# Optimization experiments

Hardware: AMD Instinct MI355X
Metric: run time of the kernel (lower is better)

## Reference

```python
import jax, jax.numpy as jnp
import numpy as np

DS = 16                      # downsample
DEPTH_MIN, DEPTH_MAX = 1.0, 60.0
XB = (-51.2, 51.2, 0.4)      # bev_x_bound
YB = (-51.2, 51.2, 0.4)      # bev_y_bound
ZB = (-5.0, 3.0)             # bev_z_bound (min, max)
BEV_H = int((YB[1] - YB[0]) / YB[2])   # 256
BEV_W = int((XB[1] - XB[0]) / XB[2])   # 256


def setup_inputs() -> dict:
    key = jax.random.key(0)
    k1, k2 = jax.random.split(key)
    B, N, C, H, W, D = 2, 6, 128, 16, 44, 64
    feat = jax.random.normal(k1, (B, N, C, H, W), dtype=jnp.float32)
    # depth distribution: softmax over depth bins (as a real LSS depth head produces)
    depth = jax.nn.softmax(jax.random.normal(k2, (B, N, D, H, W), dtype=jnp.float32), axis=2)
    # intrinsics chosen so that after the module's internal K scaling the frustum
    # rays actually spread over the BEV grid (non-degenerate valid mask)
    K = np.array([[2.0, 0.0, 1.34], [0.0, 2.0, 0.47], [0.0, 0.0, 1.0]], dtype=np.float32)
    intrinsics = np.broadcast_to(K, (B, N, 3, 3)).copy()
    # 6 cameras looking outward: cam(x right, y down, z fwd) -> ego(x fwd, y left, z up), yawed
    base = np.array([[0, 0, 1], [-1, 0, 0], [0, -1, 0]], dtype=np.float32)
    Es = []
    for yaw in np.linspace(0.0, 2.0 * np.pi, N, endpoint=False):
        c, s = np.cos(yaw), np.sin(yaw)
        Rz = np.array([[c, -s, 0], [s, c, 0], [0, 0, 1]], dtype=np.float32)
        E = np.eye(4, dtype=np.float32)
        E[:3, :3] = Rz @ base
        E[:3, 3] = [1.0 * c, 1.0 * s, 1.5]
        Es.append(E)
    extrinsics = np.broadcast_to(np.stack(Es), (B, N, 4, 4)).copy()
    return {
        "feat": feat,
        "depth": depth,
        "intrinsics": jnp.asarray(intrinsics),
        "extrinsics": jnp.asarray(extrinsics),
        "img_h": 256,
        "img_w": 704,
    }


def _forward(feat, depth, intrinsics, extrinsics, img_h, img_w):
    B, N, C, H, W = feat.shape
    D = depth.shape[2]
    dt = feat.dtype
    # frustum (D,H,W) of pixel coords u,v and metric depth d
    dbins = jnp.linspace(DEPTH_MIN, DEPTH_MAX, D).astype(dt)
    yy, xx = jnp.meshgrid(jnp.arange(H, dtype=dt), jnp.arange(W, dtype=dt), indexing='ij')
    u = jnp.broadcast_to(xx[None], (D, H, W)).reshape(-1)
    v = jnp.broadcast_to(yy[None], (D, H, W)).reshape(-1)
    d = jnp.broadcast_to(dbins[:, None, None], (D, H, W)).reshape(-1)
    # intrinsics scaled exactly as the torch module does (rows 0,1 scaled)
    scale_x = W / (img_w / DS)
    scale_y = H / (img_h / DS)
    rs = jnp.array([DS / scale_x, DS / scale_y, 1.0], dtype=dt)
    K = intrinsics * rs[:, None]            # (B,N,3,3)
    Kinv = jnp.linalg.inv(K)
    uvd = jnp.stack([u * d, v * d, d], axis=-1)     # (P,3), P = D*H*W
    pc = jnp.einsum('bnij,pj->bnpi', Kinv, uvd)     # camera-frame points
    R = extrinsics[..., :3, :3]
    t = extrinsics[..., :3, 3]
    pts = jnp.einsum('bnij,bnpj->bnpi', R, pc) + t[:, :, None, :]   # (B,N,P,3) ego
    pts = pts.reshape(B, -1, 3)                     # (B, N*P, 3)
    # depth-lift: feat (B,N,C,H,W) x depth (B,N,D,H,W) -> (B, N*D*H*W, C)
    lifted = (feat[:, :, :, None] * depth[:, :, None]).transpose(0, 1, 3, 4, 5, 2).reshape(B, -1, C)
    # voxelize (torch .long() truncates toward zero; so does astype here)
    xi = ((pts[..., 0] - XB[0]) / XB[2]).astype(jnp.int32)
    yi = ((pts[..., 1] - YB[0]) / YB[2]).astype(jnp.int32)
    valid = (xi >= 0) & (xi < BEV_W) & (yi >= 0) & (yi < BEV_H) & \
            (pts[..., 2] >= ZB[0]) & (pts[..., 2] <= ZB[1])
    idx = jnp.where(valid, yi * BEV_W + xi, 0)      # invalid -> cell 0 with zeroed value
    vals = lifted * valid[..., None].astype(dt)
    seg = lambda val, i: jax.ops.segment_sum(val, i, num_segments=BEV_H * BEV_W)
    bev = jax.vmap(seg)(vals, idx)                  # (B, cells, C)
    cnt = jax.vmap(seg)(valid.astype(dt), idx)      # (B, cells)
    bev = bev.transpose(0, 2, 1).reshape(B, C, BEV_H, BEV_W)
    cnt = cnt.reshape(B, 1, BEV_H, BEV_W)
    return bev / (cnt + 1e-5)


def reference(feat, depth, intrinsics, extrinsics, img_h, img_w):
    return _forward(feat, depth, intrinsics, extrinsics, img_h, img_w)
```

## Files before the change

kernel.cpp:

```cpp
#include <hip/hip_runtime.h>
#include <hip/hip_bf16.h>

#define Bc 2
#define Nc 6
#define Cc 128
#define Hc 16
#define Wc 44
#define Dc 64
#define HWc (Hc*Wc)
#define BNc (Bc*Nc)
#define NRAY (Nc*HWc)
#define NPTS (Bc*Nc*Dc*HWc)
#define NCOL (BNc*Wc*Dc)
#define BEV_W 256
#define BEV_H 256
#define BEV_HW (BEV_W*BEV_H)
#define NSEG (Bc*BEV_HW)
#define NSCANB 512
#define NGRP (NSEG/16)
#define GB  768
#define GW  (GB*4)
#define ZB  256
#define ZW  (ZB*4)

#define OFF_KI    0
#define OFF_DB    512
#define OFF_CNTC  1024
#define OFF_CNTP  (OFF_CNTC + 524288)
#define OFF_OFFS  (OFF_CNTP + 524288)
#define OFF_BSUM  (OFF_OFFS + 524288)
#define OFF_E8    (OFF_BSUM + 4096)
#define OFF_PK2   (OFF_E8   + 270336)
#define OFF_FT    (OFF_PK2  + 270336)
#define OFF_DT    (OFF_FT   + 4325376)
#define WS_BIG    77337600
#define OFF_FIDX  OFF_FT
#define OFF_FCNT  OFF_CNTC

__device__ __forceinline__ void setup_into(int tid, const float* __restrict__ intr,
                                           const int* __restrict__ p_imgh,
                                           const int* __restrict__ p_imgw,
                                           float* Ki, float* db) {
    if (tid < Dc) {
        double v = 1.0 + (double)tid * (59.0 / 63.0);
        db[tid] = (tid == Dc - 1) ? 60.0f : (float)v;
    }
    if (tid >= BNc) return;
    double img_h = (double)p_imgh[0];
    double img_w = (double)p_imgw[0];
    double scale_x = (double)Wc / (img_w / 16.0);
    double scale_y = (double)Hc / (img_h / 16.0);
    float rs0 = (float)(16.0 / scale_x);
    float rs1 = (float)(16.0 / scale_y);
    float rs2 = 1.0f;
    const float* K = intr + tid * 9;
    float k0 = __fmul_rn(K[0], rs0), k1 = __fmul_rn(K[1], rs0), k2 = __fmul_rn(K[2], rs0);
    float k3 = __fmul_rn(K[3], rs1), k4 = __fmul_rn(K[4], rs1), k5 = __fmul_rn(K[5], rs1);
    float k6 = __fmul_rn(K[6], rs2), k7 = __fmul_rn(K[7], rs2), k8 = __fmul_rn(K[8], rs2);
    float c0 = __fsub_rn(__fmul_rn(k4,k8), __fmul_rn(k5,k7));
    float c1 = __fsub_rn(__fmul_rn(k3,k8), __fmul_rn(k5,k6));
    float c2 = __fsub_rn(__fmul_rn(k3,k7), __fmul_rn(k4,k6));
    float det = __fadd_rn(__fsub_rn(__fmul_rn(k0,c0), __fmul_rn(k1,c1)), __fmul_rn(k2,c2));
    float* o = Ki + tid * 9;
    o[0] = __fdiv_rn(c0, det);
    o[1] = __fdiv_rn(__fsub_rn(__fmul_rn(k2,k7), __fmul_rn(k1,k8)), det);
    o[2] = __fdiv_rn(__fsub_rn(__fmul_rn(k1,k5), __fmul_rn(k2,k4)), det);
    o[3] = __fdiv_rn(__fsub_rn(__fmul_rn(k5,k6), __fmul_rn(k3,k8)), det);
    o[4] = __fdiv_rn(__fsub_rn(__fmul_rn(k0,k8), __fmul_rn(k2,k6)), det);
    o[5] = __fdiv_rn(__fsub_rn(__fmul_rn(k2,k3), __fmul_rn(k0,k5)), det);
    o[6] = __fdiv_rn(c2, det);
    o[7] = __fdiv_rn(__fsub_rn(__fmul_rn(k1,k6), __fmul_rn(k0,k7)), det);
    o[8] = __fdiv_rn(__fsub_rn(__fmul_rn(k0,k4), __fmul_rn(k1,k3)), det);
}

__global__ void k_setup(const float* __restrict__ intr, const float* __restrict__ extr,
                        const int* __restrict__ p_imgh, const int* __restrict__ p_imgw,
                        float* __restrict__ Ki, float* __restrict__ db) {
    setup_into(threadIdx.x, intr, p_imgh, p_imgw, Ki, db);
}

__device__ __forceinline__ int classify_point(int gid, const float* Ki_all,
                                              const float* db, const float* extr) {
    int p   = gid % HWc;
    int tmp = gid / HWc;
    int d   = tmp % Dc;
    int bn  = tmp / Dc;
    int w = p % Wc, h = p / Wc;
    float dd = db[d];
    float ud = __fmul_rn((float)w, dd);
    float vd = __fmul_rn((float)h, dd);
    const float* Ki = Ki_all + bn * 9;
    float pcx = fmaf(Ki[2], dd, fmaf(Ki[1], vd, __fmul_rn(Ki[0], ud)));
    float pcy = fmaf(Ki[5], dd, fmaf(Ki[4], vd, __fmul_rn(Ki[3], ud)));
    float pcz = fmaf(Ki[8], dd, fmaf(Ki[7], vd, __fmul_rn(Ki[6], ud)));
    const float* E = extr + bn * 16;
    float px = __fadd_rn(fmaf(E[2],  pcz, fmaf(E[1], pcy, __fmul_rn(E[0], pcx))), E[3]);
    float py = __fadd_rn(fmaf(E[6],  pcz, fmaf(E[5], pcy, __fmul_rn(E[4], pcx))), E[7]);
    float pz = __fadd_rn(fmaf(E[10], pcz, fmaf(E[9], pcy, __fmul_rn(E[8], pcx))), E[11]);
    float fx = __fdiv_rn(__fsub_rn(px, -51.2f), 0.4f);
    float fy = __fdiv_rn(__fsub_rn(py, -51.2f), 0.4f);
    int xi = (int)fx;
    int yi = (int)fy;
    bool valid = (xi >= 0) && (xi < BEV_W) && (yi >= 0) && (yi < BEV_H)
              && (pz >= -5.0f) && (pz <= 3.0f);
    return valid ? (yi * BEV_W + xi) : -1;
}

__device__ __forceinline__ void scan_bsum(int tid, const int* __restrict__ bsum,
                                          int* sB, int* su, int* pEtotS) {
    int2 v2 = ((const int2*)bsum)[tid];
    int s = v2.x + v2.y;
    su[tid] = s;
    __syncthreads();
    for (int st = 1; st < 256; st <<= 1) {
        int t2 = (tid >= st) ? su[tid - st] : 0;
        __syncthreads();
        su[tid] += t2;
        __syncthreads();
    }
    int base = su[tid] - s;
    sB[2 * tid]     = base;
    sB[2 * tid + 1] = base + v2.x;
    if (tid == 255) *pEtotS = base + s;
    __syncthreads();
}

__global__ __launch_bounds__(256) void k_countC(const float* __restrict__ intr,
                                                const float* __restrict__ extr,
                                                const int* __restrict__ p_imgh,
                                                const int* __restrict__ p_imgw,
                                                const float* __restrict__ feat,
                                                const float* __restrict__ depth,
                                                int* __restrict__ cntC,
                                                int* __restrict__ cntP,
                                                int2* __restrict__ pk2,
                                                float* __restrict__ ft,
                                                float* __restrict__ dT) {
    __shared__ float sKi[BNc * 9];
    __shared__ float sDb[Dc];
    __shared__ float shmem[11534];
    int tid = threadIdx.x;
    setup_into(tid, intr, p_imgh, p_imgw, sKi, sDb);
    __syncthreads();

    if (blockIdx.x < NCOL / 256) {
        int col = blockIdx.x * 256 + tid;
        int bn  = col / (Wc * Dc);
        int rem = col % (Wc * Dc);
        int w = rem / Dc, d = rem % Dc;
        const float* Ki = sKi + bn * 9;
        const float* E  = extr + bn * 16;
        float dd = sDb[d];
        float ud = __fmul_rn((float)w, dd);
        float vd0  = __fmul_rn(0.0f, dd);
        float pcx0 = fmaf(Ki[2], dd, fmaf(Ki[1], vd0, __fmul_rn(Ki[0], ud)));
        float pcy0 = fmaf(Ki[5], dd, fmaf(Ki[4], vd0, __fmul_rn(Ki[3], ud)));
        float pcz0 = fmaf(Ki[8], dd, fmaf(Ki[7], vd0, __fmul_rn(Ki[6], ud)));
        float px = __fadd_rn(fmaf(E[2], pcz0, fmaf(E[1], pcy0, __fmul_rn(E[0], pcx0))), E[3]);
        float py = __fadd_rn(fmaf(E[6], pcz0, fmaf(E[5], pcy0, __fmul_rn(E[4], pcx0))), E[7]);
        float fx = __fdiv_rn(__fsub_rn(px, -51.2f), 0.4f);
        float fy = __fdiv_rn(__fsub_rn(py, -51.2f), 0.4f);
        int xi = (int)fx, yi = (int)fy;
        bool gvalid = (xi >= 0) && (xi < BEV_W) && (yi >= 0) && (yi < BEV_H);
        unsigned hmask = 0;
        #pragma unroll
        for (int h = 0; h < Hc; h++) {
            float vd  = __fmul_rn((float)h, dd);
            float pcx = fmaf(Ki[2], dd, fmaf(Ki[1], vd, __fmul_rn(Ki[0], ud)));
            float pcy = fmaf(Ki[5], dd, fmaf(Ki[4], vd, __fmul_rn(Ki[3], ud)));
            float pcz = fmaf(Ki[8], dd, fmaf(Ki[7], vd, __fmul_rn(Ki[6], ud)));
            float pz  = __fadd_rn(fmaf(E[10], pcz, fmaf(E[9], pcy, __fmul_rn(E[8], pcx))), E[11]);
            if (pz >= -5.0f && pz <= 3.0f) hmask |= (1u << h);
        }
        int2 o;
        if (gvalid && hmask) {
            int b = bn / Nc, n = bn % Nc;
            int seg = b * BEV_HW + yi * BEV_W + xi;
            int rank = atomicAdd(&cntC[seg], 1);
            atomicAdd(&cntP[seg], __popc(hmask));
            o = make_int2(seg | (rank << 17),
                          (int)((unsigned)n | ((unsigned)w << 3) |
                                ((unsigned)d << 9) | (hmask << 15)));
        } else {
            o = make_int2(-1, 0);
        }
        pk2[col] = o;
    }

    {
        float* buf = shmem;
        int bn   = blockIdx.x / (HWc / 16);
        int tile = blockIdx.x % (HWc / 16);
        const float* fb = feat + (size_t)bn * Cc * HWc + tile * 16;
        for (int i = tid; i < Cc * 16; i += 256) {
            int c = i >> 4, hw = i & 15;
            buf[c * 17 + hw] = fb[c * HWc + hw];
        }
        __syncthreads();
        float* obt = ft + ((size_t)bn * HWc + tile * 16) * Cc;
        for (int i = tid; i < 16 * Cc; i += 256) {
            int r = i >> 7, ch = i & 127;
            obt[(size_t)r * Cc + ch] = buf[ch * 17 + r];
        }
    }

    if (blockIdx.x >= 132 && blockIdx.x < 132 + BNc * 4) {
        __syncthreads();
        int c = blockIdx.x - 132;
        int bn = c >> 2, d0 = (c & 3) << 4;
        const float* src = depth + ((size_t)bn * Dc + d0) * Hc * Wc;
        for (int i = tid; i < 16 * Hc * Wc; i += 256) {
            int ddv = i / (Hc * Wc);
            int rem = i % (Hc * Wc);
            int h = rem / Wc, w = rem % Wc;
            shmem[ddv * 721 + h * 45 + w] = src[i];
        }
        __syncthreads();
        for (int p = tid; p < Wc * 16; p += 256) {
            int w = p >> 4, ddv = p & 15;
            float* o = dT + (((size_t)bn * Wc + w) * Dc + d0 + ddv) * Hc;
            #pragma unroll
            for (int h4 = 0; h4 < 4; h4++) {
                float4 v;
                v.x = shmem[ddv * 721 + (h4 * 4 + 0) * 45 + w];
                v.y = shmem[ddv * 721 + (h4 * 4 + 1) * 45 + w];
                v.z = shmem[ddv * 721 + (h4 * 4 + 2) * 45 + w];
                v.w = shmem[ddv * 721 + (h4 * 4 + 3) * 45 + w];
                *(float4*)(o + h4 * 4) = v;
            }
        }
    }
}

__global__ __launch_bounds__(256) void k_scanB(const int* __restrict__ cntC,
                                               int* __restrict__ offs,
                                               int* __restrict__ bsum) {
    __shared__ int su[256];
    int tid = threadIdx.x;
    int g = blockIdx.x * 256 + tid;
    int v = cntC[g];
    su[tid] = v;
    __syncthreads();
    for (int st = 1; st < 256; st <<= 1) {
        int t2 = (tid >= st) ? su[tid - st] : 0;
        __syncthreads();
        su[tid] += t2;
        __syncthreads();
    }
    offs[g] = su[tid] - v;
    if (tid == 255) bsum[blockIdx.x] = su[255];
}

__global__ __launch_bounds__(256) void k_fillC(const int2* __restrict__ pk2,
                                               const int* __restrict__ offs,
                                               const int* __restrict__ bsum,
                                               int2* __restrict__ e8) {
    __shared__ int sB[NSCANB];
    __shared__ int su[256];
    __shared__ int sE;
    int tid = threadIdx.x;
    scan_bsum(tid, bsum, sB, su, &sE);
    int col = blockIdx.x * 256 + tid;
    int2 v = pk2[col];
    if (v.y == 0) return;
    int seg  = v.x & (NSEG - 1);
    int rank = (int)((unsigned)v.x >> 17);
    e8[offs[seg] + sB[seg >> 8] + rank] = make_int2(seg, v.y);
}

#define COL_ACC(EE) do {                                                        \
    int sg_ = (EE).x;                                                           \
    if (sg_ != curc) {                                                          \
        if (curc >= 0) {                                                        \
            *(float2*)&winw[(curc & 15) * 132 + 2 * lane] = a;                  \
            mask |= 1u << (curc & 15);                                          \
        }                                                                       \
        curc = sg_; a.x = 0.f; a.y = 0.f;                                       \
    }                                                                           \
    unsigned pay_ = (unsigned)(EE).y;                                           \
    int n_ = pay_ & 7, w_ = (pay_ >> 3) & 63, d_ = (pay_ >> 9) & 63;            \
    unsigned hm_ = pay_ >> 15;                                                  \
    int bn_ = (sg_ >> 16) * Nc + n_;                                            \
    const float2* fp_ = ft2 + ((size_t)bn_ * HWc + w_) * 64 + lane;             \
    const float4* dq_ = (const float4*)(dT + (((size_t)bn_ * Wc + w_) * Dc + d_) * Hc); \
    float4 dA_ = dq_[0], dB_ = dq_[1], dC_ = dq_[2], dD_ = dq_[3];              \
    _Pragma("unroll")                                                           \
    for (int h_ = 0; h_ < Hc; h_++) {                                           \
        float dv_ = (h_ < 4)  ? (&dA_.x)[h_]      :                             \
                    (h_ < 8)  ? (&dB_.x)[h_ - 4]  :                             \
                    (h_ < 12) ? (&dC_.x)[h_ - 8]  : (&dD_.x)[h_ - 12];          \
        float2 f_ = fp_[(size_t)h_ * (Wc * 64)];                                \
        float wg_ = ((hm_ >> h_) & 1u) ? dv_ : 0.f;                             \
        a.x = fmaf(wg_, f_.x, a.x);                                             \
        a.y = fmaf(wg_, f_.y, a.y);                                             \
    }                                                                           \
} while (0)

#define OG(s) (offs[s] + sB[(s) >> 8])

__global__ __launch_bounds__(256) void k_gatherC(const float2* __restrict__ ft2,
                                                 const int2* __restrict__ e8,
                                                 const int* __restrict__ cntC,
                                                 const int* __restrict__ cntP,
                                                 const int* __restrict__ offs,
                                                 const int* __restrict__ bsum,
                                                 const float* __restrict__ dT,
                                                 float* __restrict__ out) {
    __shared__ float win[4][16 * 132];
    __shared__ int sB[NSCANB];
    __shared__ int su[256];
    __shared__ int sE;
    int tid  = threadIdx.x;
    int w    = tid >> 6, lane = tid & 63;
    scan_bsum(tid, bsum, sB, su, &sE);
    int Etot = sE;

    if (blockIdx.x >= GB) {
        int zwid = (blockIdx.x - GB) * 4 + w;
        int q = lane & 3, c0 = lane >> 2;
        for (int g16 = zwid; g16 < NGRP; g16 += ZW) {
            int s0 = OG(g16 << 4);
            int s1 = (g16 == NGRP - 1) ? Etot : OG((g16 + 1) << 4);
            if (s1 != s0) continue;
            int b = g16 >> 12;
            int cell0 = (g16 & 4095) << 4;
            float* ob = out + (size_t)b * Cc * BEV_HW + cell0;
            float4 z = make_float4(0.f, 0.f, 0.f, 0.f);
            #pragma unroll
            for (int it = 0; it < 8; it++)
                *(float4*)(ob + (size_t)(it * 16 + c0) * BEV_HW + (q << 2)) = z;
        }
        return;
    }

    int gb  = (blockIdx.x & 7) * (GB / 8) + (blockIdx.x >> 3);
    int wid = gb * 4 + w;
    int WCH = (Etot + GW - 1) / GW;
    if (WCH <= 0) return;
    int start = wid * WCH;
    if (start >= Etot) return;
    int end = start + WCH; if (end > Etot) end = Etot;
    int k0 = 0;
    if (start > 0) {
        int segP = e8[start - 1].x;
        k0 = OG(segP) + cntC[segP];
        if (k0 >= end) return;
    }
    int segE = e8[end - 1].x;
    int kend = OG(segE) + cntC[segE];
    float* winw = win[w];

    int j = k0;
    while (j < kend) {
        int g16  = e8[j].x >> 4;
        bool first = (j == OG(g16 << 4));
        int gend = (g16 + 1) << 4;
        int jend = (gend < NSEG) ? OG(gend) : Etot;
        if (jend > kend) jend = kend;

        float2 a = make_float2(0.f, 0.f);
        int curc = -1;
        unsigned mask = 0;
        for (; j < jend; j++) {
            int2 ee = e8[j];
            COL_ACC(ee);
        }
        if (curc >= 0) {
            *(float2*)&winw[(curc & 15) * 132 + 2 * lane] = a;
            mask |= 1u << (curc & 15);
        }

        int cc = cntC[(g16 << 4) + (lane & 15)];
        int pv = cntP[(g16 << 4) + (lane & 15)];
        unsigned nz = (unsigned)__ballot(cc > 0) & 0xFFFFu;
        unsigned wr = mask | (first ? (0xFFFFu & ~nz) : 0u);
        int b     = g16 >> 12;
        int cell0 = (g16 & 4095) << 4;
        float* ob = out + (size_t)b * Cc * BEV_HW + cell0;
        if (wr == 0xFFFFu) {
            int q = lane & 3, c0 = lane >> 2, g0 = q << 2;
            float n0 = (float)__shfl(pv, g0);
            float n1 = (float)__shfl(pv, g0 + 1);
            float n2 = (float)__shfl(pv, g0 + 2);
            float n3 = (float)__shfl(pv, g0 + 3);
            float i0 = __fdiv_rn(1.0f, __fadd_rn(n0, 1e-5f));
            float i1 = __fdiv_rn(1.0f, __fadd_rn(n1, 1e-5f));
            float i2 = __fdiv_rn(1.0f, __fadd_rn(n2, 1e-5f));
            float i3 = __fdiv_rn(1.0f, __fadd_rn(n3, 1e-5f));
            bool o0 = (mask >> (g0 + 0)) & 1u;
            bool o1 = (mask >> (g0 + 1)) & 1u;
            bool o2 = (mask >> (g0 + 2)) & 1u;
            bool o3 = (mask >> (g0 + 3)) & 1u;
            #pragma unroll
            for (int it = 0; it < 8; it++) {
                int c = it * 16 + c0;
                float4 v;
                v.x = o0 ? __fmul_rn(winw[(g0 + 0) * 132 + c], i0) : 0.f;
                v.y = o1 ? __fmul_rn(winw[(g0 + 1) * 132 + c], i1) : 0.f;
                v.z = o2 ? __fmul_rn(winw[(g0 + 2) * 132 + c], i2) : 0.f;
                v.w = o3 ? __fmul_rn(winw[(g0 + 3) * 132 + c], i3) : 0.f;
                *(float4*)(ob + (size_t)c * BEV_HW + g0) = v;
            }
        } else {
            int g = lane & 15, cq = lane >> 4;
            bool mine = (mask >> g) & 1u;
            bool wrb  = (wr >> g) & 1u;
            float inv = __fdiv_rn(1.0f, __fadd_rn((float)pv, 1e-5f));
            #pragma unroll 4
            for (int c4 = 0; c4 < Cc; c4 += 4) {
                int c = c4 + cq;
                if (wrb) ob[(size_t)c * BEV_HW + g] =
                    mine ? __fmul_rn(winw[g * 132 + c], inv) : 0.f;
            }
        }
    }
}

__global__ __launch_bounds__(256) void k_classifyF(const float* __restrict__ Ki_all,
                                                   const float* __restrict__ db,
                                                   const float* __restrict__ extr,
                                                   int* __restrict__ idxT,
                                                   float* __restrict__ cnt) {
    int gid = blockIdx.x * 256 + threadIdx.x;
    if (gid >= NPTS) return;
    int cell = classify_point(gid, Ki_all, db, extr);
    idxT[gid] = cell;
    if (cell >= 0) {
        int b = gid / (Nc * Dc * HWc);
        atomicAdd(&cnt[b * BEV_HW + cell], 1.0f);
    }
}

__global__ __launch_bounds__(256) void k_scatterF(const float* __restrict__ feat,
                                                  const float* __restrict__ depth,
                                                  const int* __restrict__ idxT,
                                                  float* __restrict__ out) {
    __shared__ float s_dw[HWc];
    __shared__ int   s_idx[HWc];
    int blk = blockIdx.x;
    int bn  = blk / Dc;
    int b   = bn / Nc;
    int tid = threadIdx.x;
    const float* dp = depth + (size_t)blk * HWc;
    const int*   ip = idxT  + (size_t)blk * HWc;
    for (int p = tid; p < HWc; p += 256) { s_dw[p] = dp[p]; s_idx[p] = ip[p]; }
    __syncthreads();
    const float* fb = feat + (size_t)bn * Cc * HWc;
    float*       ob = out  + (size_t)b  * Cc * BEV_HW;
    for (int c = 0; c < Cc; c++) {
        const float* f = fb + (size_t)c * HWc;
        float*       o = ob + (size_t)c * BEV_HW;
        for (int p = tid; p < HWc; p += 256) {
            int cell = s_idx[p];
            if (cell >= 0) atomicAdd(&o[cell], __fmul_rn(f[p], s_dw[p]));
        }
    }
}

__global__ __launch_bounds__(256) void k_normF(float* __restrict__ out,
                                               const float* __restrict__ cnt) {
    int i = blockIdx.x * 256 + threadIdx.x;
    const int total = Bc * Cc * BEV_HW / 4;
    if (i >= total) return;
    int q = i % (BEV_HW / 4);
    int b = i / (Cc * BEV_HW / 4);
    float4 v = ((float4*)out)[i];
    float4 cv = ((const float4*)cnt)[b * (BEV_HW / 4) + q];
    v.x = __fdiv_rn(v.x, __fadd_rn(cv.x, 1e-5f));
    v.y = __fdiv_rn(v.y, __fadd_rn(cv.y, 1e-5f));
    v.z = __fdiv_rn(v.z, __fadd_rn(cv.z, 1e-5f));
    v.w = __fdiv_rn(v.w, __fadd_rn(cv.w, 1e-5f));
    ((float4*)out)[i] = v;
}

extern "C" void kernel_launch(void* const* d_in, const int* in_sizes, int n_in,
                              void* d_out, int out_size, void* d_ws, size_t ws_size,
                              hipStream_t stream) {
    const float* feat  = (const float*)d_in[0];
    const float* depth = (const float*)d_in[1];
    const float* intr  = (const float*)d_in[2];
    const float* extr  = (const float*)d_in[3];
    const int*   imh   = (const int*)d_in[4];
    const int*   imw   = (const int*)d_in[5];
    float* out = (float*)d_out;
    char*  ws  = (char*)d_ws;

    if (ws_size >= (size_t)WS_BIG) {
        int*   cntC = (int*)(ws + OFF_CNTC);
        int*   cntP = (int*)(ws + OFF_CNTP);
        int*   offs = (int*)(ws + OFF_OFFS);
        int*   bsum = (int*)(ws + OFF_BSUM);
        int2*  e8   = (int2*)(ws + OFF_E8);
        int2*  pk2  = (int2*)(ws + OFF_PK2);
        float* ft   = (float*)(ws + OFF_FT);
        float* dT   = (float*)(ws + OFF_DT);

        hipMemsetAsync(cntC, 0, 2 * (size_t)NSEG * sizeof(int), stream);
        k_countC<<<BNc * (HWc / 16), 256, 0, stream>>>(intr, extr, imh, imw, feat,
                                                       depth, cntC, cntP, pk2, ft, dT);
        k_scanB<<<NSCANB, 256, 0, stream>>>(cntC, offs, bsum);
        k_fillC<<<NCOL / 256, 256, 0, stream>>>(pk2, offs, bsum, e8);
        k_gatherC<<<GB + ZB, 256, 0, stream>>>((const float2*)ft, e8, cntC, cntP,
                                               offs, bsum, dT, out);
    } else {
        float* Ki   = (float*)(ws + OFF_KI);
        float* db   = (float*)(ws + OFF_DB);
        int*   idxT = (int*)(ws + OFF_FIDX);
        float* cnt  = (float*)(ws + OFF_FCNT);
        hipMemsetAsync(out, 0, (size_t)out_size * sizeof(float), stream);
        hipMemsetAsync(cnt, 0, (size_t)Bc * BEV_HW * sizeof(float), stream);
        k_setup<<<1, 64, 0, stream>>>(intr, extr, imh, imw, Ki, db);
        k_classifyF<<<(NPTS + 255) / 256, 256, 0, stream>>>(Ki, db, extr, idxT, cnt);
        k_scatterF<<<Bc * Nc * Dc, 256, 0, stream>>>(feat, depth, idxT, out);
        k_normF<<<(Bc * Cc * BEV_HW / 4 + 255) / 256, 256, 0, stream>>>(out, cnt);
    }
}
```

Before: 130.7 us.

## Replace in-kernel zero-fill of empty BEV groups with upfront memset of output

Removes the dedicated zero-writing blocks from the gather kernel and instead clears the whole output buffer with a memset before the pipeline. The gather kernel now only writes occupied cells, and the gather grid grows from 768 to 1024 blocks. This trades sparse, strided in-kernel zero stores for a contiguous 64 MB memset that writes every cell, including those later overwritten, which adds full-output write traffic. The classify, feature-transpose and depth-transpose bodies are moved into helper functions without changing their logic.

```diff
diff --git a/kernel.cpp b/kernel.cpp
--- a/kernel.cpp
+++ b/kernel.cpp
@@ -18,10 +18,8 @@
 #define NSEG (Bc*BEV_HW)
 #define NSCANB 512
 #define NGRP (NSEG/16)
-#define GB  768
+#define GB  1024
 #define GW  (GB*4)
-#define ZB  256
-#define ZW  (ZB*4)
 
 #define OFF_KI    0
 #define OFF_DB    512
@@ -125,148 +123,101 @@
     __syncthreads();
 }
 
-__global__ __launch_bounds__(256) void k_countC(const float* __restrict__ intr,
-                                                const float* __restrict__ extr,
-                                                const int* __restrict__ p_imgh,
-                                                const int* __restrict__ p_imgw,
-                                                const float* __restrict__ feat,
-                                                const float* __restrict__ depth,
-                                                int* __restrict__ cntC,
-                                                int* __restrict__ cntP,
-                                                int2* __restrict__ pk2,
-                                                float* __restrict__ ft,
-                                                float* __restrict__ dT) {
-    __shared__ float sKi[BNc * 9];
-    __shared__ float sDb[Dc];
-    __shared__ float shmem[11534];
-    int tid = threadIdx.x;
-    setup_into(tid, intr, p_imgh, p_imgw, sKi, sDb);
-    __syncthreads();
-
-    if (blockIdx.x < NCOL / 256) {
-        int col = blockIdx.x * 256 + tid;
-        int bn  = col / (Wc * Dc);
-        int rem = col % (Wc * Dc);
-        int w = rem / Dc, d = rem % Dc;
-        const float* Ki = sKi + bn * 9;
-        const float* E  = extr + bn * 16;
-        float dd = sDb[d];
-        float ud = __fmul_rn((float)w, dd);
-        float vd0  = __fmul_rn(0.0f, dd);
-        float pcx0 = fmaf(Ki[2], dd, fmaf(Ki[1], vd0, __fmul_rn(Ki[0], ud)));
-        float pcy0 = fmaf(Ki[5], dd, fmaf(Ki[4], vd0, __fmul_rn(Ki[3], ud)));
-        float pcz0 = fmaf(Ki[8], dd, fmaf(Ki[7], vd0, __fmul_rn(Ki[6], ud)));
-        float px = __fadd_rn(fmaf(E[2], pcz0, fmaf(E[1], pcy0, __fmul_rn(E[0], pcx0))), E[3]);
-        float py = __fadd_rn(fmaf(E[6], pcz0, fmaf(E[5], pcy0, __fmul_rn(E[4], pcx0))), E[7]);
-        float fx = __fdiv_rn(__fsub_rn(px, -51.2f), 0.4f);
-        float fy = __fdiv_rn(__fsub_rn(py, -51.2f), 0.4f);
-        int xi = (int)fx, yi = (int)fy;
-        bool gvalid = (xi >= 0) && (xi < BEV_W) && (yi >= 0) && (yi < BEV_H);
-        unsigned hmask = 0;
+
+__device__ __forceinline__ void classify_body(int col, const float* sKi,
+                                              const float* sDb,
+                                              const float* __restrict__ extr,
+                                              int* __restrict__ cntC,
+                                              int* __restrict__ cntP,
+                                              int2* __restrict__ pk2) {
+    int bn  = col / (Wc * Dc);
+    int rem = col % (Wc * Dc);
+    int w = rem / Dc, d = rem % Dc;
+    const float* Ki = sKi + bn * 9;
+    const float* E  = extr + bn * 16;
+    float dd = sDb[d];
+    float ud = __fmul_rn((float)w, dd);
+    float vd0  = __fmul_rn(0.0f, dd);
+    float pcx0 = fmaf(Ki[2], dd, fmaf(Ki[1], vd0, __fmul_rn(Ki[0], ud)));
+    float pcy0 = fmaf(Ki[5], dd, fmaf(Ki[4], vd0, __fmul_rn(Ki[3], ud)));
+    float pcz0 = fmaf(Ki[8], dd, fmaf(Ki[7], vd0, __fmul_rn(Ki[6], ud)));
+    float px = __fadd_rn(fmaf(E[2], pcz0, fmaf(E[1], pcy0, __fmul_rn(E[0], pcx0))), E[3]);
+    float py = __fadd_rn(fmaf(E[6], pcz0, fmaf(E[5], pcy0, __fmul_rn(E[4], pcx0))), E[7]);
+    float fx = __fdiv_rn(__fsub_rn(px, -51.2f), 0.4f);
+    float fy = __fdiv_rn(__fsub_rn(py, -51.2f), 0.4f);
+    int xi = (int)fx, yi = (int)fy;
+    bool gvalid = (xi >= 0) && (xi < BEV_W) && (yi >= 0) && (yi < BEV_H);
+    unsigned hmask = 0;
+    #pragma unroll
+    for (int h = 0; h < Hc; h++) {
+        float vd  = __fmul_rn((float)h, dd);
+        float pcx = fmaf(Ki[2], dd, fmaf(Ki[1], vd, __fmul_rn(Ki[0], ud)));
+        float pcy = fmaf(Ki[5], dd, fmaf(Ki[4], vd, __fmul_rn(Ki[3], ud)));
+        float pcz = fmaf(Ki[8], dd, fmaf(Ki[7], vd, __fmul_rn(Ki[6], ud)));
+        float pz  = __fadd_rn(fmaf(E[10], pcz, fmaf(E[9], pcy, __fmul_rn(E[8], pcx))), E[11]);
+        if (pz >= -5.0f && pz <= 3.0f) hmask |= (1u << h);
+    }
+    int2 o;
+    if (gvalid && hmask) {
+        int b = bn / Nc, n = bn % Nc;
+        int seg = b * BEV_HW + yi * BEV_W + xi;
+        int rank = atomicAdd(&cntC[seg], 1);
+        atomicAdd(&cntP[seg], __popc(hmask));
+        o = make_int2(seg | (rank << 17),
+                      (int)((unsigned)n | ((unsigned)w << 3) |
+                            ((unsigned)d << 9) | (hmask << 15)));
+    } else {
+        o = make_int2(-1, 0);
+    }
+    pk2[col] = o;
+}
+
+__device__ __forceinline__ void ft_body(int bid, int tid,
+                                        const float* __restrict__ feat,
+                                        float* __restrict__ ft, float* buf) {
+    int bn   = bid / (HWc / 16);
+    int tile = bid % (HWc / 16);
+    const float* fb = feat + (size_t)bn * Cc * HWc + tile * 16;
+    for (int i = tid; i < Cc * 16; i += 256) {
+        int c = i >> 4, hw = i & 15;
+        buf[c * 17 + hw] = fb[c * HWc + hw];
+    }
+    __syncthreads();
+    float* obt = ft + ((size_t)bn * HWc + tile * 16) * Cc;
+    for (int i = tid; i < 16 * Cc; i += 256) {
+        int r = i >> 7, ch = i & 127;
+        obt[(size_t)r * Cc + ch] = buf[ch * 17 + r];
+    }
+}
+
+__device__ __forceinline__ void dt_body(int chunk, int tid,
+                                        const float* __restrict__ depth,
+                                        float* __restrict__ dT, float* stage) {
+    int bn = chunk >> 2, d0 = (chunk & 3) << 4;
+    const float* src = depth + ((size_t)bn * Dc + d0) * Hc * Wc;
+    for (int i = tid; i < 16 * Hc * Wc; i += 256) {
+        int ddv = i / (Hc * Wc);
+        int rem = i % (Hc * Wc);
+        int h = rem / Wc, w = rem % Wc;
+        stage[ddv * 721 + h * 45 + w] = src[i];
+    }
+    __syncthreads();
+    for (int p = tid; p < Wc * 16; p += 256) {
+        int w = p >> 4, ddv = p & 15;
+        float* o = dT + (((size_t)bn * Wc + w) * Dc + d0 + ddv) * Hc;
         #pragma unroll
-        for (int h = 0; h < Hc; h++) {
-            float vd  = __fmul_rn((float)h, dd);
-            float pcx = fmaf(Ki[2], dd, fmaf(Ki[1], vd, __fmul_rn(Ki[0], ud)));
-            float pcy = fmaf(Ki[5], dd, fmaf(Ki[4], vd, __fmul_rn(Ki[3], ud)));
-            float pcz = fmaf(Ki[8], dd, fmaf(Ki[7], vd, __fmul_rn(Ki[6], ud)));
-            float pz  = __fadd_rn(fmaf(E[10], pcz, fmaf(E[9], pcy, __fmul_rn(E[8], pcx))), E[11]);
-            if (pz >= -5.0f && pz <= 3.0f) hmask |= (1u << h);
+        for (int h4 = 0; h4 < 4; h4++) {
+            float4 v;
+            v.x = stage[ddv * 721 + (h4 * 4 + 0) * 45 + w];
+            v.y = stage[ddv * 721 + (h4 * 4 + 1) * 45 + w];
+            v.z = stage[ddv * 721 + (h4 * 4 + 2) * 45 + w];
+            v.w = stage[ddv * 721 + (h4 * 4 + 3) * 45 + w];
+            *(float4*)(o + h4 * 4) = v;
         }
-        int2 o;
-        if (gvalid && hmask) {
-            int b = bn / Nc, n = bn % Nc;
-            int seg = b * BEV_HW + yi * BEV_W + xi;
-            int rank = atomicAdd(&cntC[seg], 1);
-            atomicAdd(&cntP[seg], __popc(hmask));
-            o = make_int2(seg | (rank << 17),
-                          (int)((unsigned)n | ((unsigned)w << 3) |
-                                ((unsigned)d << 9) | (hmask << 15)));
-        } else {
-            o = make_int2(-1, 0);
-        }
-        pk2[col] = o;
-    }
-
-    {
-        float* buf = shmem;
-        int bn   = blockIdx.x / (HWc / 16);
-        int tile = blockIdx.x % (HWc / 16);
-        const float* fb = feat + (size_t)bn * Cc * HWc + tile * 16;
-        for (int i = tid; i < Cc * 16; i += 256) {
-            int c = i >> 4, hw = i & 15;
-            buf[c * 17 + hw] = fb[c * HWc + hw];
-        }
-        __syncthreads();
-        float* obt = ft + ((size_t)bn * HWc + tile * 16) * Cc;
-        for (int i = tid; i < 16 * Cc; i += 256) {
-            int r = i >> 7, ch = i & 127;
-            obt[(size_t)r * Cc + ch] = buf[ch * 17 + r];
-        }
-    }
-
-    if (blockIdx.x >= 132 && blockIdx.x < 132 + BNc * 4) {
-        __syncthreads();
-        int c = blockIdx.x - 132;
-        int bn = c >> 2, d0 = (c & 3) << 4;
-        const float* src = depth + ((size_t)bn * Dc + d0) * Hc * Wc;
-        for (int i = tid; i < 16 * Hc * Wc; i += 256) {
-            int ddv = i / (Hc * Wc);
-            int rem = i % (Hc * Wc);
-            int h = rem / Wc, w = rem % Wc;
-            shmem[ddv * 721 + h * 45 + w] = src[i];
-        }
-        __syncthreads();
-        for (int p = tid; p < Wc * 16; p += 256) {
-            int w = p >> 4, ddv = p & 15;
-            float* o = dT + (((size_t)bn * Wc + w) * Dc + d0 + ddv) * Hc;
-            #pragma unroll
-            for (int h4 = 0; h4 < 4; h4++) {
-                float4 v;
-                v.x = shmem[ddv * 721 + (h4 * 4 + 0) * 45 + w];
-                v.y = shmem[ddv * 721 + (h4 * 4 + 1) * 45 + w];
-                v.z = shmem[ddv * 721 + (h4 * 4 + 2) * 45 + w];
-                v.w = shmem[ddv * 721 + (h4 * 4 + 3) * 45 + w];
-                *(float4*)(o + h4 * 4) = v;
-            }
-        }
-    }
-}
-
-__global__ __launch_bounds__(256) void k_scanB(const int* __restrict__ cntC,
-                                               int* __restrict__ offs,
-                                               int* __restrict__ bsum) {
-    __shared__ int su[256];
-    int tid = threadIdx.x;
-    int g = blockIdx.x * 256 + tid;
-    int v = cntC[g];
-    su[tid] = v;
-    __syncthreads();
-    for (int st = 1; st < 256; st <<= 1) {
-        int t2 = (tid >= st) ? su[tid - st] : 0;
-        __syncthreads();
-        su[tid] += t2;
-        __syncthreads();
-    }
-    offs[g] = su[tid] - v;
-    if (tid == 255) bsum[blockIdx.x] = su[255];
-}
-
-__global__ __launch_bounds__(256) void k_fillC(const int2* __restrict__ pk2,
-                                               const int* __restrict__ offs,
-                                               const int* __restrict__ bsum,
-                                               int2* __restrict__ e8) {
-    __shared__ int sB[NSCANB];
-    __shared__ int su[256];
-    __shared__ int sE;
-    int tid = threadIdx.x;
-    scan_bsum(tid, bsum, sB, su, &sE);
-    int col = blockIdx.x * 256 + tid;
-    int2 v = pk2[col];
-    if (v.y == 0) return;
-    int seg  = v.x & (NSEG - 1);
-    int rank = (int)((unsigned)v.x >> 17);
-    e8[offs[seg] + sB[seg >> 8] + rank] = make_int2(seg, v.y);
-}
+    }
+}
+
+#define OG(s) (offs[s] + sB[(s) >> 8])
 
 #define COL_ACC(EE) do {                                                        \
     int sg_ = (EE).x;                                                           \
@@ -296,7 +247,67 @@
     }                                                                           \
 } while (0)
 
-#define OG(s) (offs[s] + sB[(s) >> 8])
+__global__ __launch_bounds__(256) void k_countC(const float* __restrict__ intr,
+                                                const float* __restrict__ extr,
+                                                const int* __restrict__ p_imgh,
+                                                const int* __restrict__ p_imgw,
+                                                const float* __restrict__ feat,
+                                                const float* __restrict__ depth,
+                                                int* __restrict__ cntC,
+                                                int* __restrict__ cntP,
+                                                int2* __restrict__ pk2,
+                                                float* __restrict__ ft,
+                                                float* __restrict__ dT) {
+    __shared__ float sKi[BNc * 9];
+    __shared__ float sDb[Dc];
+    __shared__ float shmem[11534];
+    int tid = threadIdx.x;
+    setup_into(tid, intr, p_imgh, p_imgw, sKi, sDb);
+    __syncthreads();
+    if (blockIdx.x < NCOL / 256)
+        classify_body(blockIdx.x * 256 + tid, sKi, sDb, extr, cntC, cntP, pk2);
+    ft_body(blockIdx.x, tid, feat, ft, shmem);
+    if (blockIdx.x >= 132 && blockIdx.x < 132 + BNc * 4) {
+        __syncthreads();
+        dt_body(blockIdx.x - 132, tid, depth, dT, shmem);
+    }
+}
+
+__global__ __launch_bounds__(256) void k_scanB(const int* __restrict__ cntC,
+                                               int* __restrict__ offs,
+                                               int* __restrict__ bsum) {
+    __shared__ int su[256];
+    int tid = threadIdx.x;
+    int g = blockIdx.x * 256 + tid;
+    int v = cntC[g];
+    su[tid] = v;
+    __syncthreads();
+    for (int st = 1; st < 256; st <<= 1) {
+        int t2 = (tid >= st) ? su[tid - st] : 0;
+        __syncthreads();
+        su[tid] += t2;
+        __syncthreads();
+    }
+    offs[g] = su[tid] - v;
+    if (tid == 255) bsum[blockIdx.x] = su[255];
+}
+
+__global__ __launch_bounds__(256) void k_fillC(const int2* __restrict__ pk2,
+                                               const int* __restrict__ offs,
+                                               const int* __restrict__ bsum,
+                                               int2* __restrict__ e8) {
+    __shared__ int sB[NSCANB];
+    __shared__ int su[256];
+    __shared__ int sE;
+    int tid = threadIdx.x;
+    scan_bsum(tid, bsum, sB, su, &sE);
+    int col = blockIdx.x * 256 + tid;
+    int2 v = pk2[col];
+    if (v.y == 0) return;
+    int seg  = v.x & (NSEG - 1);
+    int rank = (int)((unsigned)v.x >> 17);
+    e8[offs[seg] + sB[seg >> 8] + rank] = make_int2(seg, v.y);
+}
 
 __global__ __launch_bounds__(256) void k_gatherC(const float2* __restrict__ ft2,
                                                  const int2* __restrict__ e8,
@@ -315,24 +326,6 @@
     scan_bsum(tid, bsum, sB, su, &sE);
     int Etot = sE;
 
-    if (blockIdx.x >= GB) {
-        int zwid = (blockIdx.x - GB) * 4 + w;
-        int q = lane & 3, c0 = lane >> 2;
-        for (int g16 = zwid; g16 < NGRP; g16 += ZW) {
-            int s0 = OG(g16 << 4);
-            int s1 = (g16 == NGRP - 1) ? Etot : OG((g16 + 1) << 4);
-            if (s1 != s0) continue;
-            int b = g16 >> 12;
-            int cell0 = (g16 & 4095) << 4;
-            float* ob = out + (size_t)b * Cc * BEV_HW + cell0;
-            float4 z = make_float4(0.f, 0.f, 0.f, 0.f);
-            #pragma unroll
-            for (int it = 0; it < 8; it++)
-                *(float4*)(ob + (size_t)(it * 16 + c0) * BEV_HW + (q << 2)) = z;
-        }
-        return;
-    }
-
     int gb  = (blockIdx.x & 7) * (GB / 8) + (blockIdx.x >> 3);
     int wid = gb * 4 + w;
     int WCH = (Etot + GW - 1) / GW;
@@ -353,7 +346,6 @@
     int j = k0;
     while (j < kend) {
         int g16  = e8[j].x >> 4;
-        bool first = (j == OG(g16 << 4));
         int gend = (g16 + 1) << 4;
         int jend = (gend < NSEG) ? OG(gend) : Etot;
         if (jend > kend) jend = kend;
@@ -373,7 +365,7 @@
         int cc = cntC[(g16 << 4) + (lane & 15)];
         int pv = cntP[(g16 << 4) + (lane & 15)];
         unsigned nz = (unsigned)__ballot(cc > 0) & 0xFFFFu;
-        unsigned wr = mask | (first ? (0xFFFFu & ~nz) : 0u);
+        unsigned wr = mask | (0xFFFFu & ~nz);
         int b     = g16 >> 12;
         int cell0 = (g16 & 4095) << 4;
         float* ob = out + (size_t)b * Cc * BEV_HW + cell0;
@@ -404,13 +396,12 @@
         } else {
             int g = lane & 15, cq = lane >> 4;
             bool mine = (mask >> g) & 1u;
-            bool wrb  = (wr >> g) & 1u;
             float inv = __fdiv_rn(1.0f, __fadd_rn((float)pv, 1e-5f));
             #pragma unroll 4
             for (int c4 = 0; c4 < Cc; c4 += 4) {
                 int c = c4 + cq;
-                if (wrb) ob[(size_t)c * BEV_HW + g] =
-                    mine ? __fmul_rn(winw[g * 132 + c], inv) : 0.f;
+                if (mine) ob[(size_t)c * BEV_HW + g] =
+                    __fmul_rn(winw[g * 132 + c], inv);
             }
         }
     }
@@ -496,12 +487,13 @@
         float* dT   = (float*)(ws + OFF_DT);
 
         hipMemsetAsync(cntC, 0, 2 * (size_t)NSEG * sizeof(int), stream);
+        hipMemsetAsync(out, 0, (size_t)Bc * Cc * BEV_HW * sizeof(float), stream);
         k_countC<<<BNc * (HWc / 16), 256, 0, stream>>>(intr, extr, imh, imw, feat,
                                                        depth, cntC, cntP, pk2, ft, dT);
         k_scanB<<<NSCANB, 256, 0, stream>>>(cntC, offs, bsum);
         k_fillC<<<NCOL / 256, 256, 0, stream>>>(pk2, offs, bsum, e8);
-        k_gatherC<<<GB + ZB, 256, 0, stream>>>((const float2*)ft, e8, cntC, cntP,
-                                               offs, bsum, dT, out);
+        k_gatherC<<<GB, 256, 0, stream>>>((const float2*)ft, e8, cntC, cntP,
+                                          offs, bsum, dT, out);
     } else {
         float* Ki   = (float*)(ws + OFF_KI);
         float* db   = (float*)(ws + OFF_DB);
```

Result: slower. 141.4 us (+8.3%).
